# Optimization experiments

Hardware: AMD Instinct MI355X
Metric: run time of the kernel (lower is better)

## Reference

```python
import jax, jax.numpy as jnp
import numpy as np

IMG = 768
SCORE_THR = 0.2
IOU_THR = 0.2
MAX_DET = 100  # fixed-size keep buffer (jit-compatible stand-in for dynamic keep list)


def make_anchors(img=IMG, strides=(8, 16, 32, 64, 128), anchor_scale=4.0):
    """EfficientDet anchors, y1x1y2x2 (matches Anchors module semantics)."""
    scales = (2.0 ** 0, 2.0 ** (1.0 / 3.0), 2.0 ** (2.0 / 3.0))
    ratios = ((1.0, 1.0), (1.4, 0.7), (0.7, 1.4))
    out = []
    for stride in strides:
        for s in scales:
            for rx, ry in ratios:
                base = anchor_scale * stride * s
                ax, ay = base * rx / 2.0, base * ry / 2.0
                xv = np.arange(stride / 2.0, img, stride)
                xx, yy = np.meshgrid(xv, xv)
                out.append(np.stack([yy - ay, xx - ax, yy + ay, xx + ax], -1).reshape(-1, 4))
    return np.concatenate(out, 0).astype(np.float32)  # [A,4]


def setup_inputs() -> dict:
    key = jax.random.key(0)
    k1, k2, k3 = jax.random.split(key, 3)
    A, C = 110484, 80
    x = jax.random.normal(k1, (1, 3, IMG, IMG), jnp.float32)
    regression = jax.random.normal(k2, (1, A, 4), jnp.float32) * 0.1
    classification = jax.random.normal(k3, (1, A, C), jnp.float32) - 5.0
    anchors = jnp.asarray(make_anchors())[None]  # [1,A,4]
    return {"x": x, "regression": regression, "classification": classification, "anchors": anchors}


def _decode_clip(x, regression, anchors):
    ya = (anchors[..., 0] + anchors[..., 2]) * 0.5
    xa = (anchors[..., 1] + anchors[..., 3]) * 0.5
    ha = anchors[..., 2] - anchors[..., 0]
    wa = anchors[..., 3] - anchors[..., 1]
    w = jnp.exp(regression[..., 3]) * wa
    h = jnp.exp(regression[..., 2]) * ha
    yc = regression[..., 0] * ha + ya
    xc = regression[..., 1] * wa + xa
    H, W = x.shape[2], x.shape[3]
    # ClipBoxes: x1,y1 >= 0 ; x2 <= W ; y2 <= H. Output x1y1x2y2.
    x1 = jnp.clip(xc - w * 0.5, 0.0, None)
    y1 = jnp.clip(yc - h * 0.5, 0.0, None)
    x2 = jnp.clip(xc + w * 0.5, None, float(W))
    y2 = jnp.clip(yc + h * 0.5, None, float(H))
    return jnp.stack([x1, y1, x2, y2], axis=-1)


def _nms(boxes, scores):
    """Greedy NMS. boxes [A,4] x1y1x2y2, scores [A] (-1 for below-threshold).
    Returns (keep_idx [MAX_DET] into original anchor order, keep_valid [MAX_DET])."""
    order = jnp.argsort(-scores)
    b = boxes[order]
    s = scores[order]
    area = (b[:, 2] - b[:, 0]) * (b[:, 3] - b[:, 1])
    keep_idx = jnp.zeros((MAX_DET,), jnp.int32)
    keep_valid = jnp.zeros((MAX_DET,), bool)
    active = s > 0.0

    def body(i, carry):
        active, keep_idx, keep_valid = carry
        sa = jnp.where(active, s, -1.0)
        j = jnp.argmax(sa)            # highest remaining score
        ok = sa[j] > 0.0              # any candidate left?
        keep_idx = keep_idx.at[i].set(jnp.where(ok, order[j].astype(jnp.int32), 0))
        keep_valid = keep_valid.at[i].set(ok)
        cb = b[j]
        ix1 = jnp.maximum(cb[0], b[:, 0])
        iy1 = jnp.maximum(cb[1], b[:, 1])
        ix2 = jnp.minimum(cb[2], b[:, 2])
        iy2 = jnp.minimum(cb[3], b[:, 3])
        inter = jnp.clip(ix2 - ix1, 0.0, None) * jnp.clip(iy2 - iy1, 0.0, None)
        iou = inter / (area[j] + area - inter + 1e-8)
        # torch keeps only ious < IOU_THR; current box (iou=1) is also removed
        active = active & (iou < IOU_THR) & ok
        return active, keep_idx, keep_valid

    _, keep_idx, keep_valid = jax.lax.fori_loop(0, MAX_DET, body, (active, keep_idx, keep_valid))
    return keep_idx, keep_valid


def reference(x, regression, classification, anchors):
    cls = jax.nn.sigmoid(classification)          # [1,A,C]
    boxes = _decode_clip(x, regression, anchors)  # [1,A,4]
    s = jnp.max(cls[0], axis=1)                   # per-anchor max class score
    s = jnp.where(s > SCORE_THR, s, -1.0)         # score threshold (mask instead of gather)
    keep_idx, keep_valid = _nms(boxes[0], s)
    kc = cls[0][keep_idx]                         # [MAX_DET, C]
    kscores = jnp.max(kc, axis=1)
    klabels = jnp.argmax(kc, axis=1)
    kboxes = boxes[0][keep_idx]
    v = keep_valid
    boxes_out = jnp.where(v[:, None], kboxes, 0.0)[None]   # [1,MAX_DET,4]
    scores_out = jnp.where(v, kscores, 0.0)[None]          # [1,MAX_DET]
    labels_out = jnp.where(v, klabels, 0)[None]            # [1,MAX_DET] int
    return boxes_out, scores_out, labels_out
```

## Files before the change

kernel.cpp:

```cpp
#include <hip/hip_runtime.h>
#include <hip/hip_bf16.h>

#define A_TOTAL 110484
#define NCLS 80
#define CAP 2048
#define NW 26
#define SWEEP_CAP (NW * 64)
#define MAX_DETS 100
#define IMGF 768.0f
#define IOU_T 0.2f
#define CHUNK 32

struct Ws {
    int count;
    int pad[3];
    unsigned long long key[CAP];
    float4 box[CAP];
    int label[CAP];
    unsigned long long skey[CAP];
    float4 sbox[CAP];
    int slabel[CAP];
    unsigned long long M[SWEEP_CAP * NW];
};

__global__ void score_decode_kernel(const float* __restrict__ cls,
                                    const float* __restrict__ reg,
                                    const float* __restrict__ anc,
                                    Ws* __restrict__ ws) {
    int a = blockIdx.x * blockDim.x + threadIdx.x;
    if (a >= A_TOTAL) return;

    const float4* row = (const float4*)(cls + (size_t)a * NCLS);
    float m = -1e30f;
    int lbl = 0;
#pragma unroll
    for (int i = 0; i < NCLS / 4; ++i) {
        float4 v = row[i];
        if (v.x > m) { m = v.x; lbl = i * 4 + 0; }
        if (v.y > m) { m = v.y; lbl = i * 4 + 1; }
        if (v.z > m) { m = v.z; lbl = i * 4 + 2; }
        if (v.w > m) { m = v.w; lbl = i * 4 + 3; }
    }

    float sig = 1.0f / (1.0f + expf(-m));
    if (!(sig > 0.2f)) return;

    float4 ab = ((const float4*)anc)[a];
    float4 rb = ((const float4*)reg)[a];
    float ya = __fmul_rn(__fadd_rn(ab.x, ab.z), 0.5f);
    float xa = __fmul_rn(__fadd_rn(ab.y, ab.w), 0.5f);
    float ha = __fsub_rn(ab.z, ab.x);
    float wa = __fsub_rn(ab.w, ab.y);
    float w = __fmul_rn(expf(rb.w), wa);
    float h = __fmul_rn(expf(rb.z), ha);
    float yc = __fadd_rn(__fmul_rn(rb.x, ha), ya);
    float xc = __fadd_rn(__fmul_rn(rb.y, wa), xa);
    float x1 = fmaxf(__fsub_rn(xc, __fmul_rn(w, 0.5f)), 0.0f);
    float y1 = fmaxf(__fsub_rn(yc, __fmul_rn(h, 0.5f)), 0.0f);
    float x2 = fminf(__fadd_rn(xc, __fmul_rn(w, 0.5f)), IMGF);
    float y2 = fminf(__fadd_rn(yc, __fmul_rn(h, 0.5f)), IMGF);

    int pos = atomicAdd(&ws->count, 1);
    if (pos < CAP) {
        ws->key[pos] = ((unsigned long long)__float_as_uint(sig) << 32) |
                       (unsigned int)(0xFFFFFFFFu - (unsigned int)a);
        ws->box[pos] = make_float4(x1, y1, x2, y2);
        ws->label[pos] = lbl;
    }
}

__global__ __launch_bounds__(256) void rank_kernel(Ws* __restrict__ ws) {
    __shared__ unsigned long long kl[CAP];
    int tid = threadIdx.x;
    int n = ws->count;
    if (n > CAP) n = CAP;

    for (int j = tid; j < n; j += 256) kl[j] = ws->key[j];
    __syncthreads();

    int i = blockIdx.x * 256 + tid;
    if (i >= n) return;

    unsigned long long my = kl[i];
    int r = 0;
    int j = 0;
    for (; j + 8 <= n; j += 8) {
        r += (kl[j + 0] > my) ? 1 : 0;
        r += (kl[j + 1] > my) ? 1 : 0;
        r += (kl[j + 2] > my) ? 1 : 0;
        r += (kl[j + 3] > my) ? 1 : 0;
        r += (kl[j + 4] > my) ? 1 : 0;
        r += (kl[j + 5] > my) ? 1 : 0;
        r += (kl[j + 6] > my) ? 1 : 0;
        r += (kl[j + 7] > my) ? 1 : 0;
    }
    for (; j < n; ++j) r += (kl[j] > my) ? 1 : 0;

    ws->skey[r] = my;
    ws->sbox[r] = ws->box[i];
    ws->slabel[r] = ws->label[i];
}

__global__ __launch_bounds__(256) void mask_kernel(Ws* __restrict__ ws) {
    int gw = (blockIdx.x * 256 + threadIdx.x) >> 6;
    int lane = threadIdx.x & 63;
    if (gw >= SWEEP_CAP * NW) return;
    int i = gw / NW;
    int w = gw - i * NW;
    int n = ws->count;
    if (n > CAP) n = CAP;
    if (n > SWEEP_CAP) n = SWEEP_CAP;
    if (i >= n) {
        if (lane == 0) ws->M[gw] = 0ull;
        return;
    }

    float4 kb = ws->sbox[i];
    float ka = __fmul_rn(__fsub_rn(kb.z, kb.x), __fsub_rn(kb.w, kb.y));
    int j = (w << 6) | lane;
    float4 cb = ws->sbox[j];
    float ca = __fmul_rn(__fsub_rn(cb.z, cb.x), __fsub_rn(cb.w, cb.y));
    float ix1 = fmaxf(kb.x, cb.x);
    float iy1 = fmaxf(kb.y, cb.y);
    float ix2 = fminf(kb.z, cb.z);
    float iy2 = fminf(kb.w, cb.w);
    float iw = fmaxf(__fsub_rn(ix2, ix1), 0.0f);
    float ih = fmaxf(__fsub_rn(iy2, iy1), 0.0f);
    float inter = __fmul_rn(iw, ih);
    float denom = __fadd_rn(__fadd_rn(__fadd_rn(ka, ca), -inter), 1e-8f);
    float iou = __fdiv_rn(inter, denom);
    unsigned long long bal = __ballot(!(iou < IOU_T));
    if (lane == 0) ws->M[gw] = bal;
}

__global__ __launch_bounds__(64, 1) void sweep_kernel(const Ws* __restrict__ ws,
                                                      float* __restrict__ out) {
    int lane = threadIdx.x;
    int n = ws->count;
    if (n > CAP) n = CAP;
    if (n > SWEEP_CAP) n = SWEEP_CAP;

    unsigned long long act;
    {
        int rem = n - (lane << 6);
        act = (rem >= 64) ? ~0ull : ((rem > 0) ? ((1ull << rem) - 1ull) : 0ull);
        if (lane >= NW) act = 0ull;
    }

    int k0 = 0, k1 = 0, nk = 0;

    for (int c = 0; c < SWEEP_CAP; c += CHUNK) {
        if (c >= n || nk >= MAX_DETS) break;
        unsigned long long r[CHUNK];
#pragma unroll
        for (int t = 0; t < CHUNK; ++t)
            r[t] = (lane < NW) ? ws->M[(size_t)(c + t) * NW + lane] : 0ull;
#pragma unroll
        for (int t = 0; t < CHUNK; ++t) {
            int i = c + t;
            unsigned long long aw = __shfl(act, i >> 6, 64);
            if (((aw >> (i & 63)) & 1ull) && i < n && nk < MAX_DETS) {
                if (nk < 64) { if (lane == nk) k0 = i; }
                else         { if (lane == nk - 64) k1 = i; }
                ++nk;
                act &= ~r[t];
            }
        }
    }

    for (int o = lane; o < MAX_DETS; o += 64) {
        float b0 = 0.f, b1 = 0.f, b2 = 0.f, b3 = 0.f, sc = 0.f, lb = 0.f;
        int pick = (o < 64) ? k0 : k1;
        if (o < nk) {
            float4 bb = ws->sbox[pick];
            b0 = bb.x; b1 = bb.y; b2 = bb.z; b3 = bb.w;
            sc = __uint_as_float((unsigned int)(ws->skey[pick] >> 32));
            lb = (float)ws->slabel[pick];
        }
        out[o * 4 + 0] = b0;
        out[o * 4 + 1] = b1;
        out[o * 4 + 2] = b2;
        out[o * 4 + 3] = b3;
        out[400 + o] = sc;
        out[500 + o] = lb;
    }
}

extern "C" void kernel_launch(void* const* d_in, const int* in_sizes, int n_in,
                              void* d_out, int out_size, void* d_ws, size_t ws_size,
                              hipStream_t stream) {
    const float* reg = (const float*)d_in[1];
    const float* cls = (const float*)d_in[2];
    const float* anc = (const float*)d_in[3];
    Ws* ws = (Ws*)d_ws;

    hipMemsetAsync(d_ws, 0, sizeof(int), stream);

    int blocks = (A_TOTAL + 255) / 256;
    score_decode_kernel<<<blocks, 256, 0, stream>>>(cls, reg, anc, ws);
    rank_kernel<<<CAP / 256, 256, 0, stream>>>(ws);
    mask_kernel<<<(SWEEP_CAP * NW + 3) / 4, 256, 0, stream>>>(ws);
    sweep_kernel<<<1, 64, 0, stream>>>(ws, (float*)d_out);
}
```

Measured before the change: 168.3 us.

## Split class-max across 4 lanes per anchor and skip inactive rows in sweep

The score kernel now gives each anchor four threads. Each thread scans 5 float4s of the class row, and the partial results are combined with xor shuffles on a packed, order-preserving 64-bit key that keeps the first-index tie-break. This aims to make the loads of the 35 MB classification tensor more parallel and better coalesced. The greedy NMS sweep now jumps straight to surviving boxes using readlane and ctz, and loads mask rows only for kept boxes, instead of streaming every row in chunks. The sweep becomes a serial chain of dependent global loads, one per kept detection.

New measurement: 159.7 us. 5.1% less time.

```diff
diff --git a/kernel.cpp b/kernel.cpp
--- a/kernel.cpp
+++ b/kernel.cpp
@@ -9,7 +9,6 @@
 #define MAX_DETS 100
 #define IMGF 768.0f
 #define IOU_T 0.2f
-#define CHUNK 32
 
 struct Ws {
     int count;
@@ -27,20 +26,39 @@
                                     const float* __restrict__ reg,
                                     const float* __restrict__ anc,
                                     Ws* __restrict__ ws) {
-    int a = blockIdx.x * blockDim.x + threadIdx.x;
+    int gid = blockIdx.x * blockDim.x + threadIdx.x;
+    int a = gid >> 2;
+    int sub = gid & 3;
     if (a >= A_TOTAL) return;
 
     const float4* row = (const float4*)(cls + (size_t)a * NCLS);
     float m = -1e30f;
     int lbl = 0;
 #pragma unroll
-    for (int i = 0; i < NCLS / 4; ++i) {
-        float4 v = row[i];
-        if (v.x > m) { m = v.x; lbl = i * 4 + 0; }
-        if (v.y > m) { m = v.y; lbl = i * 4 + 1; }
-        if (v.z > m) { m = v.z; lbl = i * 4 + 2; }
-        if (v.w > m) { m = v.w; lbl = i * 4 + 3; }
-    }
+    for (int q = 0; q < 5; ++q) {
+        float4 v = row[sub + q * 4];
+        int c0 = (sub + q * 4) * 4;
+        if (v.x > m) { m = v.x; lbl = c0 + 0; }
+        if (v.y > m) { m = v.y; lbl = c0 + 1; }
+        if (v.z > m) { m = v.z; lbl = c0 + 2; }
+        if (v.w > m) { m = v.w; lbl = c0 + 3; }
+    }
+
+    unsigned int mb = __float_as_uint(m);
+    mb ^= (mb & 0x80000000u) ? 0xFFFFFFFFu : 0x80000000u;
+    unsigned long long key =
+        ((unsigned long long)mb << 32) | (unsigned int)(0xFFFFFFFFu - (unsigned int)lbl);
+#pragma unroll
+    for (int d = 1; d < 4; d <<= 1) {
+        unsigned long long o = __shfl_xor(key, d, 64);
+        if (o > key) key = o;
+    }
+    if (sub != 0) return;
+
+    unsigned int hb = (unsigned int)(key >> 32);
+    hb ^= (hb & 0x80000000u) ? 0x80000000u : 0xFFFFFFFFu;
+    m = __uint_as_float(hb);
+    lbl = (int)(0xFFFFFFFFu - (unsigned int)(key & 0xFFFFFFFFu));
 
     float sig = 1.0f / (1.0f + expf(-m));
     if (!(sig > 0.2f)) return;
@@ -149,22 +167,22 @@
 
     int k0 = 0, k1 = 0, nk = 0;
 
-    for (int c = 0; c < SWEEP_CAP; c += CHUNK) {
-        if (c >= n || nk >= MAX_DETS) break;
-        unsigned long long r[CHUNK];
-#pragma unroll
-        for (int t = 0; t < CHUNK; ++t)
-            r[t] = (lane < NW) ? ws->M[(size_t)(c + t) * NW + lane] : 0ull;
-#pragma unroll
-        for (int t = 0; t < CHUNK; ++t) {
-            int i = c + t;
-            unsigned long long aw = __shfl(act, i >> 6, 64);
-            if (((aw >> (i & 63)) & 1ull) && i < n && nk < MAX_DETS) {
-                if (nk < 64) { if (lane == nk) k0 = i; }
-                else         { if (lane == nk - 64) k1 = i; }
-                ++nk;
-                act &= ~r[t];
-            }
+    for (int w = 0; w < NW && nk < MAX_DETS; ++w) {
+        unsigned int lo = __builtin_amdgcn_readlane((unsigned int)(act & 0xFFFFFFFFull), w);
+        unsigned int hi = __builtin_amdgcn_readlane((unsigned int)(act >> 32), w);
+        unsigned long long aw = ((unsigned long long)hi << 32) | lo;
+        while (aw) {
+            int b = __builtin_ctzll(aw);
+            int i = (w << 6) | b;
+            if (nk < 64) { if (lane == nk) k0 = i; }
+            else         { if (lane == nk - 64) k1 = i; }
+            ++nk;
+            if (nk >= MAX_DETS) break;
+            unsigned long long rowm = (lane < NW) ? ws->M[(size_t)i * NW + lane] : 0ull;
+            act &= ~rowm;
+            lo = __builtin_amdgcn_readlane((unsigned int)(act & 0xFFFFFFFFull), w);
+            hi = __builtin_amdgcn_readlane((unsigned int)(act >> 32), w);
+            aw = (((unsigned long long)hi << 32) | lo) & ~((2ull << b) - 1ull);
         }
     }
 
@@ -196,7 +214,7 @@
 
     hipMemsetAsync(d_ws, 0, sizeof(int), stream);
 
-    int blocks = (A_TOTAL + 255) / 256;
+    int blocks = (A_TOTAL * 4 + 255) / 256;
     score_decode_kernel<<<blocks, 256, 0, stream>>>(cls, reg, anc, ws);
     rank_kernel<<<CAP / 256, 256, 0, stream>>>(ws);
     mask_kernel<<<(SWEEP_CAP * NW + 3) / 4, 256, 0, stream>>>(ws);
```
